# Performance work log

Hardware: AMD Instinct MI355X
Metric: run time of the kernel (lower is better)

Reference implementation:

```python
import jax, jax.numpy as jnp
import numpy as np

EPS = 1e-5  # torch BatchNorm default


def setup_inputs() -> dict:
    key = jax.random.key(0)
    ks = jax.random.split(key, 8)
    B, Q, S, C = 4, 256, 128, 256
    feats = [2 * C, 256, 64, 1]  # opt['num_features']
    inp = {
        "support_features": jax.random.normal(ks[0], (B, S, C), dtype=jnp.float32),
        "query_features": jax.random.normal(ks[1], (B, Q, C), dtype=jnp.float32),
    }
    for i in range(3):
        fan_in, fan_out = feats[i], feats[i + 1]
        std = np.sqrt(2.0 / (fan_in + fan_out))  # xavier_normal on conv weight
        inp[f"W{i}"] = jax.random.normal(ks[2 + i], (fan_out, fan_in), dtype=jnp.float32) * std
        inp[f"b{i}"] = jnp.zeros((fan_out,), dtype=jnp.float32)
        inp[f"g{i}"] = jnp.ones((fan_out,), dtype=jnp.float32)   # BN weight
        inp[f"bt{i}"] = jnp.zeros((fan_out,), dtype=jnp.float32)  # BN bias
    return inp


def _bn_relu(x, g, bt):
    # x: [B, N, C]; BatchNorm1d training-mode stats over batch and length dims
    mean = jnp.mean(x, axis=(0, 1))
    var = jnp.mean(jnp.square(x - mean), axis=(0, 1))  # biased var, as torch BN
    return jax.nn.relu((x - mean) * (g * jax.lax.rsqrt(var + EPS)) + bt)


def reference(support_features, query_features,
              W0, b0, g0, bt0, W1, b1, g1, bt1, W2, b2, g2, bt2):
    B, S, C = support_features.shape
    Q = query_features.shape[1]
    # pairwise concat: [B, Q, S, 2C]
    uq = jnp.broadcast_to(query_features[:, :, None, :], (B, Q, S, C))
    us = jnp.broadcast_to(support_features[:, None, :, :], (B, Q, S, C))
    x = jnp.concatenate([uq, us], axis=3).reshape(B, Q * S, 2 * C)
    # 1x1 conv == matmul over channel dim
    x = _bn_relu(jnp.einsum('bnc,oc->bno', x, W0) + b0, g0, bt0)
    x = _bn_relu(jnp.einsum('bnc,oc->bno', x, W1) + b1, g1, bt1)
    x = _bn_relu(jnp.einsum('bnc,oc->bno', x, W2) + b2, g2, bt2)
    # back to [B, C_out, Q, S]
    return jnp.transpose(x, (0, 2, 1)).reshape(B, -1, Q, S)
```

## Files before the change

### kernel.cpp

```cpp
#include <hip/hip_runtime.h>
#include <hip/hip_bf16.h>


typedef __attribute__((ext_vector_type(4))) float f32x4;
typedef __attribute__((ext_vector_type(8))) short s16x8;

#define BN_EPS 1e-5f
#define INV_N  (1.0f/131072.0f)

#define LEAFA(g)   ((g)*16)
#define ROOTA      512
#define GATEA(g)   (528 + (g)*16)
#define LEAFB(g)   (1040 + (g)*16)
#define ROOTB      1552
#define GATEB(g)   (1568 + (g)*16)
#define CNT_ZERO   2080

__device__ __forceinline__ unsigned pk_bf16(float a, float b) {
  float2 t; t.x = a; t.y = b;
  __hip_bfloat162 h = __float22bfloat162_rn(t);
  return *reinterpret_cast<unsigned*>(&h);
}
__device__ __forceinline__ void split2(float a, float b, unsigned& uh, unsigned& ul) {
  uh = pk_bf16(a, b);
  float ha = __uint_as_float(uh << 16);
  float hb = __uint_as_float(uh & 0xFFFF0000u);
  ul = pk_bf16(a - ha, b - hb);
}

__device__ __forceinline__ unsigned a_ld(const unsigned* p) {
  return __hip_atomic_load(p, __ATOMIC_RELAXED, __HIP_MEMORY_SCOPE_AGENT);
}
__device__ __forceinline__ float a_ldf(const float* p) {
  return __hip_atomic_load(p, __ATOMIC_RELAXED, __HIP_MEMORY_SCOPE_AGENT);
}
__device__ __forceinline__ void a_st(unsigned* p, unsigned v) {
  __hip_atomic_store(p, v, __ATOMIC_RELAXED, __HIP_MEMORY_SCOPE_AGENT);
}
__device__ __forceinline__ void a_stf(float* p, float v) {
  __hip_atomic_store(p, v, __ATOMIC_RELAXED, __HIP_MEMORY_SCOPE_AGENT);
}
__device__ __forceinline__ unsigned a_add(unsigned* p) {
  return __hip_atomic_fetch_add(p, 1u, __ATOMIC_RELAXED, __HIP_MEMORY_SCOPE_AGENT);
}

union frag_u { s16x8 v; unsigned u[4]; };

struct Args {
  const float *Sf, *Qf, *W0, *b0, *g0, *bt0, *W1, *b1, *g1, *bt1, *W2, *b2, *g2, *bt2;
  float *Aq, *As, *ws0s, *ws1p, *ws1g, *ws1r, *ws2p, *ws2g, *out;
  unsigned *cnt;
};

__global__ __launch_bounds__(64) void k_g0(Args a)
{
  int bi = blockIdx.x, t = threadIdx.x;
  if (bi == 384) {
    for (int i = t; i < CNT_ZERO; i += 64) a.cnt[i] = 0u;
    return;
  }
  int l15 = t & 15, quad = t >> 4;
  int chunk = bi >> 2, ntile = bi & 3;
  bool isQ = (chunk < 64);
  const float* X; float* Out; int m0, koff;
  if (isQ) { m0 = chunk * 16; X = a.Qf; Out = a.Aq; koff = 0; }
  else     { m0 = (chunk - 64) * 16; X = a.Sf; Out = a.As; koff = 256; }
  int n0 = ntile * 64;

  f32x4 acc[4] = {};
#pragma unroll
  for (int ko = 0; ko < 256; ko += 32) {
    const float* row = X + (m0 + l15) * 256 + ko + quad * 8;
    f32x4 v0 = *(const f32x4*)(row);
    f32x4 v1 = *(const f32x4*)(row + 4);
    frag_u ah, al;
#pragma unroll
    for (int j = 0; j < 2; j++) {
      split2(v0[2 * j], v0[2 * j + 1], ah.u[j], al.u[j]);
      split2(v1[2 * j], v1[2 * j + 1], ah.u[2 + j], al.u[2 + j]);
    }
#pragma unroll
    for (int nt = 0; nt < 4; nt++) {
      const float* wrow = a.W0 + (n0 + nt * 16 + l15) * 512 + koff + ko + quad * 8;
      f32x4 w0v = *(const f32x4*)(wrow);
      f32x4 w1v = *(const f32x4*)(wrow + 4);
      frag_u bh, bl;
      split2(w0v[0], w0v[1], bh.u[0], bl.u[0]);
      split2(w0v[2], w0v[3], bh.u[1], bl.u[1]);
      split2(w1v[0], w1v[1], bh.u[2], bl.u[2]);
      split2(w1v[2], w1v[3], bh.u[3], bl.u[3]);
      acc[nt] = __builtin_amdgcn_mfma_f32_16x16x32_bf16(ah.v, bh.v, acc[nt], 0, 0, 0);
      acc[nt] = __builtin_amdgcn_mfma_f32_16x16x32_bf16(al.v, bh.v, acc[nt], 0, 0, 0);
      acc[nt] = __builtin_amdgcn_mfma_f32_16x16x32_bf16(ah.v, bl.v, acc[nt], 0, 0, 0);
    }
  }
#pragma unroll
  for (int nt = 0; nt < 4; nt++) {
    int o = n0 + nt * 16 + l15;
    float bias = isQ ? 0.0f : a.b0[o];
    float cs = 0, cs2 = 0;
#pragma unroll
    for (int r = 0; r < 4; r++) {
      float y = acc[nt][r] + bias;
      Out[(m0 + quad * 4 + r) * 256 + o] = y;
      cs += y; cs2 += y * y;
    }
    cs  += __shfl_xor(cs, 16);  cs  += __shfl_xor(cs, 32);
    cs2 += __shfl_xor(cs2, 16); cs2 += __shfl_xor(cs2, 32);
    if (quad == 0) {
      a.ws0s[chunk * 512 + o] = cs;
      a.ws0s[chunk * 512 + 256 + o] = cs2;
    }
  }
}

__device__ __forceinline__ void bn0_finalize(const Args& a, int t, float* sh_a0c0)
{
  int o = t;
  float sumY = 0, cross = 0, SQ2 = 0, SS2 = 0;
#pragma unroll
  for (int b = 0; b < 4; b++) {
    float sq1 = 0, sq2 = 0, ss1 = 0, ss2 = 0;
#pragma unroll
    for (int c = 0; c < 16; c++) {
      sq1 += a.ws0s[(b * 16 + c) * 512 + o];
      sq2 += a.ws0s[(b * 16 + c) * 512 + 256 + o];
    }
#pragma unroll
    for (int c = 0; c < 8; c++) {
      ss1 += a.ws0s[(64 + b * 8 + c) * 512 + o];
      ss2 += a.ws0s[(64 + b * 8 + c) * 512 + 256 + o];
    }
    SQ2 += sq2; SS2 += ss2;
    sumY += 128.0f * sq1 + 256.0f * ss1;
    cross += sq1 * ss1;
  }
  float mean = sumY * INV_N;
  float var = (128.0f * SQ2 + 256.0f * SS2 + 2.0f * cross) * INV_N - mean * mean;
  float aa = a.g0[o] * rsqrtf(var + BN_EPS);
  sh_a0c0[o] = aa;
  sh_a0c0[256 + o] = a.bt0[o] - mean * aa;
}

__global__ __launch_bounds__(256, 2) void k_f(Args a)
{
  int bi = blockIdx.x, t = threadIdx.x;
  int w = t >> 6, l = t & 63, l15 = l & 15, quad = l >> 4;
  __shared__ ushort w1f[2048 * 8];
  __shared__ float sh_a0c0[512];
  __shared__ float red[2][4][4][16];
  __shared__ float sh_tot[128];
  __shared__ float sh_a1c1[128];
  __shared__ float rs[16], rs2[16];
  __shared__ float sh_fin[2];
  __shared__ int s_role;

#pragma unroll
  for (int i = 0; i < 8; i++) {
    int fr = i * 256 + t;
    int kk = fr >> 8, r = fr & 255, nt = r >> 6, ln = r & 63;
    const float* src = a.W1 + (nt * 16 + (ln & 15)) * 256 + kk * 32 + (ln >> 4) * 8;
    f32x4 v0 = *(const f32x4*)(src);
    f32x4 v1 = *(const f32x4*)(src + 4);
    frag_u z;
    z.u[0] = pk_bf16(v0[0], v0[1]); z.u[1] = pk_bf16(v0[2], v0[3]);
    z.u[2] = pk_bf16(v1[0], v1[1]); z.u[3] = pk_bf16(v1[2], v1[3]);
    *(s16x8*)(w1f + fr * 8) = z.v;
  }
  bn0_finalize(a, t, sh_a0c0);
  __syncthreads();

  int b_ = bi >> 7, rem = bi & 127, qt = rem >> 3, st = rem & 7;
  const float* asrow = a.As + ((b_ << 7) + st * 16 + l15) * 256;
  const float* aqrow[4];
#pragma unroll
  for (int mt = 0; mt < 4; mt++)
    aqrow[mt] = a.Aq + ((b_ << 8) + qt * 16 + w * 4 + mt) * 256;

  f32x4 acc[4][4] = {};
#pragma unroll
  for (int kk = 0; kk < 8; kk++) {
    int obase = kk * 32 + quad * 8;
    f32x4 a0v0 = *(const f32x4*)(sh_a0c0 + obase);
    f32x4 a0v1 = *(const f32x4*)(sh_a0c0 + obase + 4);
    f32x4 c0v0 = *(const f32x4*)(sh_a0c0 + 256 + obase);
    f32x4 c0v1 = *(const f32x4*)(sh_a0c0 + 256 + obase + 4);
    f32x4 as0 = *(const f32x4*)(asrow + obase);
    f32x4 as1 = *(const f32x4*)(asrow + obase + 4);

    s16x8 zh[4];
#pragma unroll
    for (int mt = 0; mt < 4; mt++) {
      f32x4 aq0 = *(const f32x4*)(aqrow[mt] + obase);
      f32x4 aq1 = *(const f32x4*)(aqrow[mt] + obase + 4);
      f32x4 z0 = (aq0 + as0) * a0v0 + c0v0;
      f32x4 z1 = (aq1 + as1) * a0v1 + c0v1;
      frag_u zz;
      zz.u[0] = pk_bf16(fmaxf(z0[0], 0.0f), fmaxf(z0[1], 0.0f));
      zz.u[1] = pk_bf16(fmaxf(z0[2], 0.0f), fmaxf(z0[3], 0.0f));
      zz.u[2] = pk_bf16(fmaxf(z1[0], 0.0f), fmaxf(z1[1], 0.0f));
      zz.u[3] = pk_bf16(fmaxf(z1[2], 0.0f), fmaxf(z1[3], 0.0f));
      zh[mt] = zz.v;
    }
#pragma unroll
    for (int nt = 0; nt < 4; nt++) {
      s16x8 bw = *(const s16x8*)(w1f + ((kk * 4 + nt) * 64 + l) * 8);
#pragma unroll
      for (int mt = 0; mt < 4; mt++)
        acc[mt][nt] = __builtin_amdgcn_mfma_f32_16x16x32_bf16(zh[mt], bw, acc[mt][nt], 0, 0, 0);
    }
  }

  float biasv[4];
#pragma unroll
  for (int nt = 0; nt < 4; nt++) biasv[nt] = a.b1[nt * 16 + l15];
  unsigned ku01[4][4], ku23[4][4];
  float s[4] = {0, 0, 0, 0}, s2[4] = {0, 0, 0, 0};
#pragma unroll
  for (int mt = 0; mt < 4; mt++) {
#pragma unroll
    for (int nt = 0; nt < 4; nt++) {
      float y0 = acc[mt][nt][0] + biasv[nt];
      float y1 = acc[mt][nt][1] + biasv[nt];
      float y2v = acc[mt][nt][2] + biasv[nt];
      float y3 = acc[mt][nt][3] + biasv[nt];
      unsigned u01 = pk_bf16(y0, y1), u23 = pk_bf16(y2v, y3);
      ku01[mt][nt] = u01; ku23[mt][nt] = u23;
      float f0 = __uint_as_float(u01 << 16), f1 = __uint_as_float(u01 & 0xFFFF0000u);
      float f2 = __uint_as_float(u23 << 16), f3 = __uint_as_float(u23 & 0xFFFF0000u);
      s[nt]  += f0 + f1 + f2 + f3;
      s2[nt] += f0 * f0 + f1 * f1 + f2 * f2 + f3 * f3;
    }
  }
#pragma unroll
  for (int nt = 0; nt < 4; nt++) {
    float v = s[nt], v2 = s2[nt];
    v  += __shfl_xor(v, 16);  v  += __shfl_xor(v, 32);
    v2 += __shfl_xor(v2, 16); v2 += __shfl_xor(v2, 32);
    if (quad == 0) { red[0][w][nt][l15] = v; red[1][w][nt][l15] = v2; }
  }
  __syncthreads();
  if (t < 128) {
    int which = t >> 6, j = t & 63, nt = j >> 4, jl = j & 15;
    float v = red[which][0][nt][jl] + red[which][1][nt][jl] +
              red[which][2][nt][jl] + red[which][3][nt][jl];
    a_stf(&a.ws1p[bi * 128 + t], v);
  }

  asm volatile("s_waitcnt vmcnt(0)" ::: "memory");
  __syncthreads();
  int g = bi & 31;
  if (t == 0) {
    unsigned old = a_add(&a.cnt[LEAFA(g)]);
    s_role = (old == 15u) ? 1 : 0;
  }
  __syncthreads();
  if (s_role) {
    if (t < 128) {
      float sum = 0;
#pragma unroll
      for (int c = 0; c < 16; c++)
        sum += a_ldf(&a.ws1p[(g + c * 32) * 128 + t]);
      a_stf(&a.ws1g[g * 128 + t], sum);
    }
    asm volatile("s_waitcnt vmcnt(0)" ::: "memory");
    __syncthreads();
    if (t == 0) {
      unsigned r = a_add(&a.cnt[ROOTA]);
      s_role = (r == 31u) ? 2 : 1;
    }
    __syncthreads();
    if (s_role == 2) {
      if (t < 128) {
        float tot = 0;
#pragma unroll
        for (int gg = 0; gg < 32; gg++)
          tot += a_ldf(&a.ws1g[gg * 128 + t]);
        sh_tot[t] = tot;
      }
      __syncthreads();
      if (t < 64) {
        float mean = sh_tot[t] * INV_N;
        float var = sh_tot[64 + t] * INV_N - mean * mean;
        float aa = a.g1[t] * rsqrtf(var + BN_EPS);
        sh_a1c1[t] = aa;
        sh_a1c1[64 + t] = a.bt1[t] - mean * aa;
      }
      __syncthreads();
      if (t < 128) {
        float uv = sh_a1c1[t];
#pragma unroll
        for (int r2 = 0; r2 < 32; r2++)
          a_stf(&a.ws1r[r2 * 128 + t], uv);
      }
      asm volatile("s_waitcnt vmcnt(0)" ::: "memory");
      __syncthreads();
      if (t == 0) {
#pragma unroll
        for (int i = 0; i < 32; i++) a_st(&a.cnt[GATEA(i)], 1u);
      }
    }
  }
  if (t == 0) {
    while (a_ld(&a.cnt[GATEA(g)]) == 0u) __builtin_amdgcn_s_sleep(32);
  }
  __syncthreads();
  if (t < 128)
    sh_a1c1[t] = a_ldf(&a.ws1r[g * 128 + t]);
  __syncthreads();

  float a1v[4], c1v[4], w2v[4];
#pragma unroll
  for (int nt = 0; nt < 4; nt++) {
    int j = nt * 16 + l15;
    a1v[nt] = sh_a1c1[j]; c1v[nt] = sh_a1c1[64 + j]; w2v[nt] = a.W2[j];
  }
  float b2v = a.b2[0];
  float y2k[4][4];
  float ls = 0, ls2 = 0;
#pragma unroll
  for (int mt = 0; mt < 4; mt++) {
    float part[4] = {0, 0, 0, 0};
#pragma unroll
    for (int nt = 0; nt < 4; nt++) {
      unsigned u01 = ku01[mt][nt], u23 = ku23[mt][nt];
      float f0 = __uint_as_float(u01 << 16), f1 = __uint_as_float(u01 & 0xFFFF0000u);
      float f2 = __uint_as_float(u23 << 16), f3 = __uint_as_float(u23 & 0xFFFF0000u);
      part[0] += fmaxf(a1v[nt] * f0 + c1v[nt], 0.0f) * w2v[nt];
      part[1] += fmaxf(a1v[nt] * f1 + c1v[nt], 0.0f) * w2v[nt];
      part[2] += fmaxf(a1v[nt] * f2 + c1v[nt], 0.0f) * w2v[nt];
      part[3] += fmaxf(a1v[nt] * f3 + c1v[nt], 0.0f) * w2v[nt];
    }
#pragma unroll
    for (int r = 0; r < 4; r++) {
      float pv = part[r];
      pv += __shfl_xor(pv, 1); pv += __shfl_xor(pv, 2);
      pv += __shfl_xor(pv, 4); pv += __shfl_xor(pv, 8);
      float y = pv + b2v;
      y2k[mt][r] = y;
      if (l15 == 0) { ls += y; ls2 += y * y; }
    }
  }
  if (l15 == 0) { rs[t >> 4] = ls; rs2[t >> 4] = ls2; }
  __syncthreads();
  if (t == 0) {
    float sv = 0, sv2 = 0;
#pragma unroll
    for (int i = 0; i < 16; i++) { sv += rs[i]; sv2 += rs2[i]; }
    a_stf(&a.ws2p[bi * 2], sv);
    a_stf(&a.ws2p[bi * 2 + 1], sv2);
  }

  asm volatile("s_waitcnt vmcnt(0)" ::: "memory");
  __syncthreads();
  if (t == 0) {
    unsigned old = a_add(&a.cnt[LEAFB(g)]);
    if (old == 15u) {
      float s0 = 0, s1 = 0;
#pragma unroll
      for (int c = 0; c < 16; c++) {
        int m = g + c * 32;
        s0 += a_ldf(&a.ws2p[m * 2]);
        s1 += a_ldf(&a.ws2p[m * 2 + 1]);
      }
      a_stf(&a.ws2g[g * 2], s0);
      a_stf(&a.ws2g[g * 2 + 1], s1);
      asm volatile("s_waitcnt vmcnt(0)" ::: "memory");
      unsigned r = a_add(&a.cnt[ROOTB]);
      if (r == 31u) {
        float sv = 0, sv2 = 0;
#pragma unroll
        for (int gg = 0; gg < 32; gg++) {
          sv  += a_ldf(&a.ws2g[gg * 2]);
          sv2 += a_ldf(&a.ws2g[gg * 2 + 1]);
        }
        float mean = sv * INV_N;
        float var = sv2 * INV_N - mean * mean;
        float aa = a.g2[0] * rsqrtf(var + BN_EPS);
        float cc = a.bt2[0] - mean * aa;
        unsigned ua = __float_as_uint(aa), uc = __float_as_uint(cc);
#pragma unroll
        for (int i = 0; i < 32; i++) {
          a_st(&a.cnt[GATEB(i) + 1], ua);
          a_st(&a.cnt[GATEB(i) + 2], uc);
        }
        asm volatile("s_waitcnt vmcnt(0)" ::: "memory");
#pragma unroll
        for (int i = 0; i < 32; i++) a_st(&a.cnt[GATEB(i)], 1u);
      }
    }
    while (a_ld(&a.cnt[GATEB(g)]) == 0u) __builtin_amdgcn_s_sleep(32);
    sh_fin[0] = __uint_as_float(a_ld(&a.cnt[GATEB(g) + 1]));
    sh_fin[1] = __uint_as_float(a_ld(&a.cnt[GATEB(g) + 2]));
  }
  __syncthreads();
  float aav = sh_fin[0], ccv = sh_fin[1];

#pragma unroll
  for (int mt = 0; mt < 4; mt++) {
    if (l15 == 0) {
      int q = qt * 16 + w * 4 + mt;
      int P = ((b_ * 256 + q) * 128) + st * 16 + quad * 4;
      f32x4 o;
#pragma unroll
      for (int r = 0; r < 4; r++) o[r] = fmaxf(aav * y2k[mt][r] + ccv, 0.0f);
      *(f32x4*)(a.out + P) = o;
    }
  }
}

extern "C" void kernel_launch(void* const* d_in, const int* in_sizes, int n_in,
                              void* d_out, int out_size, void* d_ws, size_t ws_size,
                              hipStream_t stream)
{
  float* ws = (float*)d_ws;
  Args a;
  a.Sf  = (const float*)d_in[0];
  a.Qf  = (const float*)d_in[1];
  a.W0  = (const float*)d_in[2];
  a.b0  = (const float*)d_in[3];
  a.g0  = (const float*)d_in[4];
  a.bt0 = (const float*)d_in[5];
  a.W1  = (const float*)d_in[6];
  a.b1  = (const float*)d_in[7];
  a.g1  = (const float*)d_in[8];
  a.bt1 = (const float*)d_in[9];
  a.W2  = (const float*)d_in[10];
  a.b2  = (const float*)d_in[11];
  a.g2  = (const float*)d_in[12];
  a.bt2 = (const float*)d_in[13];

  a.Aq   = ws;
  a.As   = ws + 262144;
  a.ws0s = ws + 524288;
  a.ws1p = ws + 573440;
  a.ws1g = ws + 638976;
  a.ws1r = ws + 643072;
  a.ws2p = ws + 647168;
  a.ws2g = ws + 648192;
  a.cnt  = (unsigned*)(ws + 648256);
  a.out  = (float*)d_out;

  k_g0<<<385, 64, 0, stream>>>(a);
  k_f <<<512, 256, 0, stream>>>(a);
}
```

Before: 125.7 us.

## Replace in-kernel grid barrier for final BatchNorm with a separate output kernel

The last BatchNorm previously used a two-level atomic counter tree and a spin-wait gate inside the fused kernel, so every block had to wait for the global statistics before writing its output. Now the fused kernel writes the pre-normalisation layer-2 values and the per-block partial sums to workspace and exits. A new small kernel reduces the 512 partials, computes the scale and shift, and applies the affine-plus-ReLU over the whole output. This removes the spin-wait and atomic traffic at the end of the main kernel, at the cost of an extra launch and a round trip of the output-sized buffer through global memory.

```diff
diff --git a/kernel.cpp b/kernel.cpp
--- a/kernel.cpp
+++ b/kernel.cpp
@@ -11,10 +11,7 @@
 #define LEAFA(g)   ((g)*16)
 #define ROOTA      512
 #define GATEA(g)   (528 + (g)*16)
-#define LEAFB(g)   (1040 + (g)*16)
-#define ROOTB      1552
-#define GATEB(g)   (1568 + (g)*16)
-#define CNT_ZERO   2080
+#define CNT_ZERO   1040
 
 __device__ __forceinline__ unsigned pk_bf16(float a, float b) {
   float2 t; t.x = a; t.y = b;
@@ -48,7 +45,7 @@
 
 struct Args {
   const float *Sf, *Qf, *W0, *b0, *g0, *bt0, *W1, *b1, *g1, *bt1, *W2, *b2, *g2, *bt2;
-  float *Aq, *As, *ws0s, *ws1p, *ws1g, *ws1r, *ws2p, *ws2g, *out;
+  float *Aq, *As, *y2, *ws0s, *ws1p, *ws1g, *ws1r, *ws2p, *out;
   unsigned *cnt;
 };
 
@@ -152,7 +149,6 @@
   __shared__ float sh_tot[128];
   __shared__ float sh_a1c1[128];
   __shared__ float rs[16], rs2[16];
-  __shared__ float sh_fin[2];
   __shared__ int s_role;
 
 #pragma unroll
@@ -316,7 +312,6 @@
     a1v[nt] = sh_a1c1[j]; c1v[nt] = sh_a1c1[64 + j]; w2v[nt] = a.W2[j];
   }
   float b2v = a.b2[0];
-  float y2k[4][4];
   float ls = 0, ls2 = 0;
 #pragma unroll
   for (int mt = 0; mt < 4; mt++) {
@@ -331,82 +326,61 @@
       part[2] += fmaxf(a1v[nt] * f2 + c1v[nt], 0.0f) * w2v[nt];
       part[3] += fmaxf(a1v[nt] * f3 + c1v[nt], 0.0f) * w2v[nt];
     }
+    f32x4 o;
 #pragma unroll
     for (int r = 0; r < 4; r++) {
       float pv = part[r];
       pv += __shfl_xor(pv, 1); pv += __shfl_xor(pv, 2);
       pv += __shfl_xor(pv, 4); pv += __shfl_xor(pv, 8);
       float y = pv + b2v;
-      y2k[mt][r] = y;
+      o[r] = y;
       if (l15 == 0) { ls += y; ls2 += y * y; }
     }
-  }
-  if (l15 == 0) { rs[t >> 4] = ls; rs2[t >> 4] = ls2; }
-  __syncthreads();
-  if (t == 0) {
-    float sv = 0, sv2 = 0;
-#pragma unroll
-    for (int i = 0; i < 16; i++) { sv += rs[i]; sv2 += rs2[i]; }
-    a_stf(&a.ws2p[bi * 2], sv);
-    a_stf(&a.ws2p[bi * 2 + 1], sv2);
-  }
-
-  asm volatile("s_waitcnt vmcnt(0)" ::: "memory");
-  __syncthreads();
-  if (t == 0) {
-    unsigned old = a_add(&a.cnt[LEAFB(g)]);
-    if (old == 15u) {
-      float s0 = 0, s1 = 0;
-#pragma unroll
-      for (int c = 0; c < 16; c++) {
-        int m = g + c * 32;
-        s0 += a_ldf(&a.ws2p[m * 2]);
-        s1 += a_ldf(&a.ws2p[m * 2 + 1]);
-      }
-      a_stf(&a.ws2g[g * 2], s0);
-      a_stf(&a.ws2g[g * 2 + 1], s1);
-      asm volatile("s_waitcnt vmcnt(0)" ::: "memory");
-      unsigned r = a_add(&a.cnt[ROOTB]);
-      if (r == 31u) {
-        float sv = 0, sv2 = 0;
-#pragma unroll
-        for (int gg = 0; gg < 32; gg++) {
-          sv  += a_ldf(&a.ws2g[gg * 2]);
-          sv2 += a_ldf(&a.ws2g[gg * 2 + 1]);
-        }
-        float mean = sv * INV_N;
-        float var = sv2 * INV_N - mean * mean;
-        float aa = a.g2[0] * rsqrtf(var + BN_EPS);
-        float cc = a.bt2[0] - mean * aa;
-        unsigned ua = __float_as_uint(aa), uc = __float_as_uint(cc);
-#pragma unroll
-        for (int i = 0; i < 32; i++) {
-          a_st(&a.cnt[GATEB(i) + 1], ua);
-          a_st(&a.cnt[GATEB(i) + 2], uc);
-        }
-        asm volatile("s_waitcnt vmcnt(0)" ::: "memory");
-#pragma unroll
-        for (int i = 0; i < 32; i++) a_st(&a.cnt[GATEB(i)], 1u);
-      }
-    }
-    while (a_ld(&a.cnt[GATEB(g)]) == 0u) __builtin_amdgcn_s_sleep(32);
-    sh_fin[0] = __uint_as_float(a_ld(&a.cnt[GATEB(g) + 1]));
-    sh_fin[1] = __uint_as_float(a_ld(&a.cnt[GATEB(g) + 2]));
-  }
-  __syncthreads();
-  float aav = sh_fin[0], ccv = sh_fin[1];
-
-#pragma unroll
-  for (int mt = 0; mt < 4; mt++) {
     if (l15 == 0) {
       int q = qt * 16 + w * 4 + mt;
       int P = ((b_ * 256 + q) * 128) + st * 16 + quad * 4;
-      f32x4 o;
-#pragma unroll
-      for (int r = 0; r < 4; r++) o[r] = fmaxf(aav * y2k[mt][r] + ccv, 0.0f);
-      *(f32x4*)(a.out + P) = o;
-    }
-  }
+      *(f32x4*)(a.y2 + P) = o;
+    }
+  }
+  if (l15 == 0) { rs[t >> 4] = ls; rs2[t >> 4] = ls2; }
+  __syncthreads();
+  if (t == 0) {
+    float sv = 0, sv2 = 0;
+#pragma unroll
+    for (int i = 0; i < 16; i++) { sv += rs[i]; sv2 += rs2[i]; }
+    a.ws2p[bi * 2] = sv;
+    a.ws2p[bi * 2 + 1] = sv2;
+  }
+}
+
+__global__ __launch_bounds__(256) void k_out(Args a)
+{
+  int t = threadIdx.x;
+  __shared__ float wsum[4], wsum2[4];
+  __shared__ float fin[2];
+  f32x4 v = *(const f32x4*)(a.ws2p + t * 4);
+  float s = v[0] + v[2], s2 = v[1] + v[3];
+#pragma unroll
+  for (int d = 1; d < 64; d <<= 1) { s += __shfl_xor(s, d); s2 += __shfl_xor(s2, d); }
+  if ((t & 63) == 0) { wsum[t >> 6] = s; wsum2[t >> 6] = s2; }
+  __syncthreads();
+  if (t == 0) {
+    float sv  = wsum[0] + wsum[1] + wsum[2] + wsum[3];
+    float sv2 = wsum2[0] + wsum2[1] + wsum2[2] + wsum2[3];
+    float mean = sv * INV_N;
+    float var = sv2 * INV_N - mean * mean;
+    float aa = a.g2[0] * rsqrtf(var + BN_EPS);
+    fin[0] = aa;
+    fin[1] = a.bt2[0] - mean * aa;
+  }
+  __syncthreads();
+  float aa = fin[0], cc = fin[1];
+  int i = (blockIdx.x * 256 + t) * 4;
+  f32x4 y = *(const f32x4*)(a.y2 + i);
+  f32x4 o;
+#pragma unroll
+  for (int r = 0; r < 4; r++) o[r] = fmaxf(aa * y[r] + cc, 0.0f);
+  *(f32x4*)(a.out + i) = o;
 }
 
 extern "C" void kernel_launch(void* const* d_in, const int* in_sizes, int n_in,
@@ -432,15 +406,16 @@
 
   a.Aq   = ws;
   a.As   = ws + 262144;
+  a.y2   = ws + 393216;
   a.ws0s = ws + 524288;
   a.ws1p = ws + 573440;
   a.ws1g = ws + 638976;
   a.ws1r = ws + 643072;
   a.ws2p = ws + 647168;
-  a.ws2g = ws + 648192;
-  a.cnt  = (unsigned*)(ws + 648256);
+  a.cnt  = (unsigned*)(ws + 648192);
   a.out  = (float*)d_out;
 
-  k_g0<<<385, 64, 0, stream>>>(a);
-  k_f <<<512, 256, 0, stream>>>(a);
-}
+  k_g0 <<<385, 64, 0, stream>>>(a);
+  k_f  <<<512, 256, 0, stream>>>(a);
+  k_out<<<128, 256, 0, stream>>>(a);
+}
```

Result: no change. 123.8 us, median of 2 (-1.5%).

## Fuse layer-0 GEMM kernel into main kernel with sentinel-based grid barrier

Applied to the files above, without the earlier changes.

The separate layer-0 projection kernel is folded into the main persistent kernel. Each wave computes one 16x16 output tile, then all blocks meet at a two-level grid barrier that uses 64-bit sentinel values, so the barrier needs no zeroed counters. Removing the second launch cuts launch overhead and the gap between kernels. In exchange it relies on all 512 blocks being co-resident, adds spin-wait time, and depends on the sentinel never appearing in stale workspace memory.

```diff
diff --git a/kernel.cpp b/kernel.cpp
--- a/kernel.cpp
+++ b/kernel.cpp
@@ -14,7 +14,13 @@
 #define LEAFB(g)   (1040 + (g)*16)
 #define ROOTB      1552
 #define GATEB(g)   (1568 + (g)*16)
-#define CNT_ZERO   2080
+#define CNT_ZN     2080
+#define ARR0(b)    (2080 + (b)*16)
+#define GRP0(g)    (10272 + (g)*16)
+#define GATE0(g)   (10784 + (g)*16)
+#define CNT_TOT    11296
+
+#define SENT 0x9BDF024613572468ull
 
 __device__ __forceinline__ unsigned pk_bf16(float a, float b) {
   float2 t; t.x = a; t.y = b;
@@ -43,6 +49,12 @@
 __device__ __forceinline__ unsigned a_add(unsigned* p) {
   return __hip_atomic_fetch_add(p, 1u, __ATOMIC_RELAXED, __HIP_MEMORY_SCOPE_AGENT);
 }
+__device__ __forceinline__ unsigned long long a_ld64(const unsigned long long* p) {
+  return __hip_atomic_load(p, __ATOMIC_RELAXED, __HIP_MEMORY_SCOPE_AGENT);
+}
+__device__ __forceinline__ void a_st64(unsigned long long* p, unsigned long long v) {
+  __hip_atomic_store(p, v, __ATOMIC_RELAXED, __HIP_MEMORY_SCOPE_AGENT);
+}
 
 union frag_u { s16x8 v; unsigned u[4]; };
 
@@ -52,68 +64,6 @@
   unsigned *cnt;
 };
 
-__global__ __launch_bounds__(64) void k_g0(Args a)
-{
-  int bi = blockIdx.x, t = threadIdx.x;
-  if (bi == 384) {
-    for (int i = t; i < CNT_ZERO; i += 64) a.cnt[i] = 0u;
-    return;
-  }
-  int l15 = t & 15, quad = t >> 4;
-  int chunk = bi >> 2, ntile = bi & 3;
-  bool isQ = (chunk < 64);
-  const float* X; float* Out; int m0, koff;
-  if (isQ) { m0 = chunk * 16; X = a.Qf; Out = a.Aq; koff = 0; }
-  else     { m0 = (chunk - 64) * 16; X = a.Sf; Out = a.As; koff = 256; }
-  int n0 = ntile * 64;
-
-  f32x4 acc[4] = {};
-#pragma unroll
-  for (int ko = 0; ko < 256; ko += 32) {
-    const float* row = X + (m0 + l15) * 256 + ko + quad * 8;
-    f32x4 v0 = *(const f32x4*)(row);
-    f32x4 v1 = *(const f32x4*)(row + 4);
-    frag_u ah, al;
-#pragma unroll
-    for (int j = 0; j < 2; j++) {
-      split2(v0[2 * j], v0[2 * j + 1], ah.u[j], al.u[j]);
-      split2(v1[2 * j], v1[2 * j + 1], ah.u[2 + j], al.u[2 + j]);
-    }
-#pragma unroll
-    for (int nt = 0; nt < 4; nt++) {
-      const float* wrow = a.W0 + (n0 + nt * 16 + l15) * 512 + koff + ko + quad * 8;
-      f32x4 w0v = *(const f32x4*)(wrow);
-      f32x4 w1v = *(const f32x4*)(wrow + 4);
-      frag_u bh, bl;
-      split2(w0v[0], w0v[1], bh.u[0], bl.u[0]);
-      split2(w0v[2], w0v[3], bh.u[1], bl.u[1]);
-      split2(w1v[0], w1v[1], bh.u[2], bl.u[2]);
-      split2(w1v[2], w1v[3], bh.u[3], bl.u[3]);
-      acc[nt] = __builtin_amdgcn_mfma_f32_16x16x32_bf16(ah.v, bh.v, acc[nt], 0, 0, 0);
-      acc[nt] = __builtin_amdgcn_mfma_f32_16x16x32_bf16(al.v, bh.v, acc[nt], 0, 0, 0);
-      acc[nt] = __builtin_amdgcn_mfma_f32_16x16x32_bf16(ah.v, bl.v, acc[nt], 0, 0, 0);
-    }
-  }
-#pragma unroll
-  for (int nt = 0; nt < 4; nt++) {
-    int o = n0 + nt * 16 + l15;
-    float bias = isQ ? 0.0f : a.b0[o];
-    float cs = 0, cs2 = 0;
-#pragma unroll
-    for (int r = 0; r < 4; r++) {
-      float y = acc[nt][r] + bias;
-      Out[(m0 + quad * 4 + r) * 256 + o] = y;
-      cs += y; cs2 += y * y;
-    }
-    cs  += __shfl_xor(cs, 16);  cs  += __shfl_xor(cs, 32);
-    cs2 += __shfl_xor(cs2, 16); cs2 += __shfl_xor(cs2, 32);
-    if (quad == 0) {
-      a.ws0s[chunk * 512 + o] = cs;
-      a.ws0s[chunk * 512 + 256 + o] = cs2;
-    }
-  }
-}
-
 __device__ __forceinline__ void bn0_finalize(const Args& a, int t, float* sh_a0c0)
 {
   int o = t;
@@ -142,7 +92,7 @@
   sh_a0c0[256 + o] = a.bt0[o] - mean * aa;
 }
 
-__global__ __launch_bounds__(256, 2) void k_f(Args a)
+__global__ __launch_bounds__(256, 2) void k_all(Args a)
 {
   int bi = blockIdx.x, t = threadIdx.x;
   int w = t >> 6, l = t & 63, l15 = l & 15, quad = l >> 4;
@@ -154,6 +104,88 @@
   __shared__ float rs[16], rs2[16];
   __shared__ float sh_fin[2];
   __shared__ int s_role;
+
+  int gw = bi * 4 + w;
+  if (gw < 1536) {
+    int chunk = gw >> 4, nt16 = gw & 15;
+    bool isQ = (chunk < 64);
+    const float* X; float* OutP; int m0, koff;
+    if (isQ) { m0 = chunk * 16; X = a.Qf; OutP = a.Aq; koff = 0; }
+    else     { m0 = (chunk - 64) * 16; X = a.Sf; OutP = a.As; koff = 256; }
+    int o0 = nt16 * 16;
+
+    f32x4 acc0 = {};
+#pragma unroll
+    for (int ko = 0; ko < 256; ko += 32) {
+      const float* row = X + (m0 + l15) * 256 + ko + quad * 8;
+      f32x4 v0 = *(const f32x4*)(row);
+      f32x4 v1 = *(const f32x4*)(row + 4);
+      frag_u ah, al;
+#pragma unroll
+      for (int j = 0; j < 2; j++) {
+        split2(v0[2 * j], v0[2 * j + 1], ah.u[j], al.u[j]);
+        split2(v1[2 * j], v1[2 * j + 1], ah.u[2 + j], al.u[2 + j]);
+      }
+      const float* wrow = a.W0 + (o0 + l15) * 512 + koff + ko + quad * 8;
+      f32x4 w0v = *(const f32x4*)(wrow);
+      f32x4 w1v = *(const f32x4*)(wrow + 4);
+      frag_u bh, bl;
+      split2(w0v[0], w0v[1], bh.u[0], bl.u[0]);
+      split2(w0v[2], w0v[3], bh.u[1], bl.u[1]);
+      split2(w1v[0], w1v[1], bh.u[2], bl.u[2]);
+      split2(w1v[2], w1v[3], bh.u[3], bl.u[3]);
+      acc0 = __builtin_amdgcn_mfma_f32_16x16x32_bf16(ah.v, bh.v, acc0, 0, 0, 0);
+      acc0 = __builtin_amdgcn_mfma_f32_16x16x32_bf16(al.v, bh.v, acc0, 0, 0, 0);
+      acc0 = __builtin_amdgcn_mfma_f32_16x16x32_bf16(ah.v, bl.v, acc0, 0, 0, 0);
+    }
+    int o = o0 + l15;
+    float bias = isQ ? 0.0f : a.b0[o];
+    float cs = 0, cs2 = 0;
+#pragma unroll
+    for (int r = 0; r < 4; r++) {
+      float y = acc0[r] + bias;
+      a_stf(&OutP[(m0 + quad * 4 + r) * 256 + o], y);
+      cs += y; cs2 += y * y;
+    }
+    cs  += __shfl_xor(cs, 16);  cs  += __shfl_xor(cs, 32);
+    cs2 += __shfl_xor(cs2, 16); cs2 += __shfl_xor(cs2, 32);
+    if (quad == 0) {
+      a_stf(&a.ws0s[chunk * 512 + o], cs);
+      a_stf(&a.ws0s[chunk * 512 + 256 + o], cs2);
+    }
+  }
+  if (bi >= 496) {
+    int zidx = (bi - 496) * 256 + t;
+    if (zidx < CNT_ZN) a_st(&a.cnt[zidx], 0u);
+  }
+
+  asm volatile("s_waitcnt vmcnt(0)" ::: "memory");
+  __syncthreads();
+  {
+    unsigned long long* C64 = (unsigned long long*)a.cnt;
+    if (t == 0) {
+      a_st64(&C64[ARR0(bi) / 2], SENT);
+      if (bi < 32) {
+#pragma unroll 1
+        for (int c = 0; c < 16; c++)
+          while (a_ld64(&C64[ARR0(bi + 32 * c) / 2]) != SENT)
+            __builtin_amdgcn_s_sleep(8);
+        a_st64(&C64[GRP0(bi) / 2], SENT);
+      }
+      if (bi == 0) {
+#pragma unroll 1
+        for (int g2 = 0; g2 < 32; g2++)
+          while (a_ld64(&C64[GRP0(g2) / 2]) != SENT)
+            __builtin_amdgcn_s_sleep(8);
+#pragma unroll 1
+        for (int g2 = 0; g2 < 32; g2++) a_st64(&C64[GATE0(g2) / 2], SENT);
+      }
+      while (a_ld64(&C64[GATE0(bi & 31) / 2]) != SENT)
+        __builtin_amdgcn_s_sleep(8);
+    }
+    __syncthreads();
+    __builtin_amdgcn_fence(__ATOMIC_ACQUIRE, "agent");
+  }
 
 #pragma unroll
   for (int i = 0; i < 8; i++) {
@@ -441,6 +473,5 @@
   a.cnt  = (unsigned*)(ws + 648256);
   a.out  = (float*)d_out;
 
-  k_g0<<<385, 64, 0, stream>>>(a);
-  k_f <<<512, 256, 0, stream>>>(a);
-}
+  k_all<<<512, 256, 0, stream>>>(a);
+}
```

Measured after the change: 149.1 us. 18.6% more time.
